# Optimization experiments

Measured on AMD Instinct MI355X. Metric: run time of the kernel, lower is better.

Reference implementation:

```python
import jax, jax.numpy as jnp
import numpy as np

NC, NS, NX, NZ = 128, 2048, 256, 512
B, K = 4, 1
NNZ = NX * NZ * NC  # 16_777_216 nonzeros (~Nc contributions per pixel)


def setup_inputs() -> dict:
    key = jax.random.key(0)
    k1, k2, k3, k4 = jax.random.split(key, 4)
    x = jax.random.normal(k1, (B, K, NC, NS), dtype=jnp.float32)
    csr_vals = jax.random.normal(k2, (NNZ,), dtype=jnp.float32)
    csr_rows = jnp.sort(jax.random.randint(k3, (NNZ,), 0, NX * NZ, dtype=jnp.int64))
    csr_cols = jax.random.randint(k4, (NNZ,), 0, NS * NC, dtype=jnp.int64)
    return {"x": x, "csr_vals": csr_vals, "csr_rows": csr_rows, "csr_cols": csr_cols}


def reference(x, csr_vals, csr_rows, csr_cols):
    # (B,K,Nc,Ns) -> (B,K,Ns,Nc) -> (B*K, Ns*Nc) -> transpose -> (Ns*Nc, B*K)
    rhs = jnp.transpose(x, (0, 1, 3, 2)).reshape(B * K, NS * NC).T
    # SpMM in COO form: out[r, :] += vals * rhs[cols, :]
    gathered = csr_vals[:, None] * rhs[csr_cols]          # (nnz, B*K)
    img_vec = jax.ops.segment_sum(gathered, csr_rows, num_segments=NX * NZ)  # (Nx*Nz, B*K)
    # transpose -> (B*K, Nx*Nz) -> (B,K,Nx,Nz) -> (B,K,Nz,Nx)
    return jnp.transpose(img_vec.T.reshape(B, K, NX, NZ), (0, 1, 3, 2))
```

## Files before the change

### kernel.cpp

```cpp
#include <hip/hip_runtime.h>
#include <hip/hip_fp16.h>

#define NC 128
#define NS 2048
#define NX 256
#define NZ 512
#define NROWS (NX * NZ)
#define NCOLS (NS * NC)
#define RUN 16
#define WAVE_NNZ (RUN * 64)
#define NSLOTS 64


struct alignas(8) Half4 { __half2 lo, hi; };

__global__ void pack_rhs_kernel(const float* __restrict__ x,
                                Half4* __restrict__ rhs) {
    int j = blockIdx.x * blockDim.x + threadIdx.x;
    if (j >= NCOLS) return;
    int c = j >> 11;
    int s = j & (NS - 1);
    int base = c * NS + s;
    Half4 h;
    h.lo = __float22half2_rn(make_float2(x[base],               x[base + 1 * NC * NS]));
    h.hi = __float22half2_rn(make_float2(x[base + 2 * NC * NS], x[base + 3 * NC * NS]));
    rhs[s * NC + c] = h;
}

__device__ __forceinline__ void global_flush(float* __restrict__ out, int r, float4 a) {
    int ix = r >> 9;
    int iz = r & (NZ - 1);
    int o = iz * NX + ix;
    atomicAdd(&out[0 * NROWS + o], a.x);
    atomicAdd(&out[1 * NROWS + o], a.y);
    atomicAdd(&out[2 * NROWS + o], a.z);
    atomicAdd(&out[3 * NROWS + o], a.w);
}

__global__ void __launch_bounds__(256, 4) spmm_seg_kernel(
        const float* __restrict__ vals,
        const int* __restrict__ cols,
        const int* __restrict__ rows,
        const Half4* __restrict__ rhs,
        float* __restrict__ out,
        int nnz) {
    __shared__ float sl[4][NSLOTS][4];

    int wv   = threadIdx.x >> 6;
    int lane = threadIdx.x & 63;
    int wid  = (blockIdx.x << 2) + wv;
    int base = wid * WAVE_NNZ + lane * RUN;

    ((float4*)sl)[threadIdx.x] = make_float4(0.f, 0.f, 0.f, 0.f);
    __syncthreads();

    float4 v[4];
    int4   c4[4], r4[4];
    if (base + RUN <= nnz) {
        #pragma unroll
        for (int q = 0; q < 4; ++q) c4[q] = *(const int4*)(cols + base + 4 * q);
        #pragma unroll
        for (int q = 0; q < 4; ++q) v[q]  = *(const float4*)(vals + base + 4 * q);
        #pragma unroll
        for (int q = 0; q < 4; ++q) r4[q] = *(const int4*)(rows + base + 4 * q);
    } else {
        #pragma unroll
        for (int q = 0; q < 4; ++q) {
            #pragma unroll
            for (int k = 0; k < 4; ++k) {
                int e = base + 4 * q + k;
                int ec = e < nnz ? e : (nnz - 1);
                (&v[q].x)[k]  = e < nnz ? vals[ec] : 0.f;
                (&c4[q].x)[k] = cols[ec];
                (&r4[q].x)[k] = rows[ec];
            }
        }
    }

    Half4 g[RUN];
    #pragma unroll
    for (int q = 0; q < 4; ++q) {
        g[4 * q + 0] = rhs[c4[q].x];
        g[4 * q + 1] = rhs[c4[q].y];
        g[4 * q + 2] = rhs[c4[q].z];
        g[4 * q + 3] = rhs[c4[q].w];
    }
    __builtin_amdgcn_sched_barrier(0);

    int rfirst = __shfl(r4[0].x, 0);
    int rlast  = __shfl(r4[3].w, 63);

    int cur = r4[0].x;
    float4 acc = make_float4(0.f, 0.f, 0.f, 0.f);
    #pragma unroll
    for (int j = 0; j < RUN; ++j) {
        int   rj = (&r4[j >> 2].x)[j & 3];
        float vj = (&v[j >> 2].x)[j & 3];
        float2 lo = __half22float2(g[j].lo);
        float2 hi = __half22float2(g[j].hi);
        if (rj != cur) {
            int s = cur - rfirst;
            if (s < NSLOTS) {
                atomicAdd(&sl[wv][s][0], acc.x);
                atomicAdd(&sl[wv][s][1], acc.y);
                atomicAdd(&sl[wv][s][2], acc.z);
                atomicAdd(&sl[wv][s][3], acc.w);
            } else {
                global_flush(out, cur, acc);
            }
            acc = make_float4(0.f, 0.f, 0.f, 0.f);
            cur = rj;
        }
        acc.x += vj * lo.x;
        acc.y += vj * lo.y;
        acc.z += vj * hi.x;
        acc.w += vj * hi.y;
    }
    {
        int s = cur - rfirst;
        if (s < NSLOTS) {
            atomicAdd(&sl[wv][s][0], acc.x);
            atomicAdd(&sl[wv][s][1], acc.y);
            atomicAdd(&sl[wv][s][2], acc.z);
            atomicAdd(&sl[wv][s][3], acc.w);
        } else {
            global_flush(out, cur, acc);
        }
    }

    __syncthreads();

    int span = rlast - rfirst;
    if (lane <= span && lane < NSLOTS) {
        float ax = sl[wv][lane][0];
        float ay = sl[wv][lane][1];
        float az = sl[wv][lane][2];
        float aw = sl[wv][lane][3];
        int rr = rfirst + lane;
        int ix = rr >> 9;
        int iz = rr & (NZ - 1);
        int o = iz * NX + ix;
        if (lane == 0 || rr == rlast) {
            atomicAdd(&out[0 * NROWS + o], ax);
            atomicAdd(&out[1 * NROWS + o], ay);
            atomicAdd(&out[2 * NROWS + o], az);
            atomicAdd(&out[3 * NROWS + o], aw);
        } else {
            out[0 * NROWS + o] = ax;
            out[1 * NROWS + o] = ay;
            out[2 * NROWS + o] = az;
            out[3 * NROWS + o] = aw;
        }
    }
}

__global__ void __launch_bounds__(256) spmm_direct_kernel(
        const float* __restrict__ x,
        const float* __restrict__ vals,
        const int* __restrict__ rows,
        const int* __restrict__ cols,
        int nnz,
        float* __restrict__ out) {
    int r = (blockIdx.x << 2) + (threadIdx.x >> 6);
    int lane = threadIdx.x & 63;
    int start, end;
    {
        int lo = 0, hi = nnz;
        while (lo < hi) { int mid = (lo + hi) >> 1; if (rows[mid] < r) lo = mid + 1; else hi = mid; }
        start = lo;
        hi = nnz;
        int key = r + 1;
        while (lo < hi) { int mid = (lo + hi) >> 1; if (rows[mid] < key) lo = mid + 1; else hi = mid; }
        end = lo;
    }
    float4 acc = {0.f, 0.f, 0.f, 0.f};
    for (int i = start + lane; i < end; i += 64) {
        float v = vals[i];
        int col = cols[i];
        int cc = col & (NC - 1);
        int ss = col >> 7;
        int b = cc * NS + ss;
        acc.x += v * x[b];
        acc.y += v * x[b + 1 * NC * NS];
        acc.z += v * x[b + 2 * NC * NS];
        acc.w += v * x[b + 3 * NC * NS];
    }
    #pragma unroll
    for (int off = 32; off >= 1; off >>= 1) {
        acc.x += __shfl_xor(acc.x, off, 64);
        acc.y += __shfl_xor(acc.y, off, 64);
        acc.z += __shfl_xor(acc.z, off, 64);
        acc.w += __shfl_xor(acc.w, off, 64);
    }
    if (lane < 4) {
        float o = (lane == 0) ? acc.x : (lane == 1) ? acc.y : (lane == 2) ? acc.z : acc.w;
        int ix = r >> 9;
        int iz = r & (NZ - 1);
        out[lane * NROWS + iz * NX + ix] = o;
    }
}

extern "C" void kernel_launch(void* const* d_in, const int* in_sizes, int n_in,
                              void* d_out, int out_size, void* d_ws, size_t ws_size,
                              hipStream_t stream) {
    const float* x        = (const float*)d_in[0];
    const float* csr_vals = (const float*)d_in[1];
    const int*   csr_rows = (const int*)d_in[2];
    const int*   csr_cols = (const int*)d_in[3];
    float* out = (float*)d_out;
    int nnz = in_sizes[1];

    size_t need = (size_t)NCOLS * sizeof(Half4);
    if (ws_size >= need) {
        Half4* rhs = (Half4*)d_ws;
        hipMemsetAsync(out, 0, (size_t)out_size * sizeof(float), stream);
        pack_rhs_kernel<<<(NCOLS + 255) / 256, 256, 0, stream>>>(x, rhs);
        int nblocks = (nnz + 4 * WAVE_NNZ - 1) / (4 * WAVE_NNZ);
        spmm_seg_kernel<<<nblocks, 256, 0, stream>>>(csr_vals, csr_cols, csr_rows,
                                                     rhs, out, nnz);
    } else {
        spmm_direct_kernel<<<NROWS / 4, 256, 0, stream>>>(x, csr_vals, csr_rows, csr_cols, nnz, out);
    }
}
```

Measured before the change: 283.3 us.

## Software-pipeline SpMM gathers across four tiles per wave with inline-asm loads

```diff
diff --git a/kernel.cpp b/kernel.cpp
--- a/kernel.cpp
+++ b/kernel.cpp
@@ -7,12 +7,36 @@
 #define NZ 512
 #define NROWS (NX * NZ)
 #define NCOLS (NS * NC)
-#define RUN 16
-#define WAVE_NNZ (RUN * 64)
+#define RUN 8
+#define TILE_NNZ (RUN * 64)
+#define NT 4
+#define WAVE_RANGE (NT * TILE_NNZ)
 #define NSLOTS 64
 
 
 struct alignas(8) Half4 { __half2 lo, hi; };
+
+typedef int   vi4 __attribute__((ext_vector_type(4)));
+typedef float vf4 __attribute__((ext_vector_type(4)));
+
+__device__ __forceinline__ void ld4i(vi4& d, const int* p) {
+    asm volatile("global_load_dwordx4 %0, %1, off"
+                 : "=v"(d) : "v"((unsigned long long)p));
+}
+__device__ __forceinline__ void ld4f(vf4& d, const float* p) {
+    asm volatile("global_load_dwordx4 %0, %1, off"
+                 : "=v"(d) : "v"((unsigned long long)p));
+}
+__device__ __forceinline__ void ld1i(int& d, const int* p) {
+    asm volatile("global_load_dword %0, %1, off"
+                 : "=v"(d) : "v"((unsigned long long)p));
+}
+__device__ __forceinline__ void ld2u(unsigned long long& d, const Half4* p) {
+    asm volatile("global_load_dwordx2 %0, %1, off"
+                 : "=v"(d) : "v"((unsigned long long)p));
+}
+#define WAITV(n) do { asm volatile("s_waitcnt vmcnt(" #n ")" ::: "memory"); \
+                      __builtin_amdgcn_sched_barrier(0); } while (0)
 
 __global__ void pack_rhs_kernel(const float* __restrict__ x,
                                 Half4* __restrict__ rhs) {
@@ -37,7 +61,55 @@
     atomicAdd(&out[3 * NROWS + o], a.w);
 }
 
-__global__ void __launch_bounds__(256, 4) spmm_seg_kernel(
+__device__ __forceinline__ void flush_slot(float (*slw)[4], int rfirst, int cur,
+                                           float4 acc, float* __restrict__ out) {
+    int s = cur - rfirst;
+    if (s < NSLOTS) {
+        atomicAdd(&slw[s][0], acc.x);
+        atomicAdd(&slw[s][1], acc.y);
+        atomicAdd(&slw[s][2], acc.z);
+        atomicAdd(&slw[s][3], acc.w);
+    } else {
+        global_flush(out, cur, acc);
+    }
+}
+
+__device__ __forceinline__ void accum8(const vf4& va, const vf4& vb,
+                                       const vi4& ra, const vi4& rb,
+                                       const unsigned long long (&g)[8],
+                                       int rfirst, int& cur, float4& acc,
+                                       float* __restrict__ out, float (*slw)[4]) {
+    #pragma unroll
+    for (int j = 0; j < 8; ++j) {
+        int   rj = (j < 4) ? ra[j] : rb[j - 4];
+        float vj = (j < 4) ? va[j] : vb[j - 4];
+        union { unsigned long long u; Half4 h; } u; u.u = g[j];
+        float2 lo = __half22float2(u.h.lo);
+        float2 hi = __half22float2(u.h.hi);
+        if (rj != cur) {
+            flush_slot(slw, rfirst, cur, acc, out);
+            acc = make_float4(0.f, 0.f, 0.f, 0.f);
+            cur = rj;
+        }
+        acc.x += vj * lo.x;
+        acc.y += vj * lo.y;
+        acc.z += vj * hi.x;
+        acc.w += vj * hi.y;
+    }
+}
+
+#define ISSUE_S(cx0, cx1, vx0, vx1, rx0, rx1, b) do { \
+    ld4i(cx0, cols + (b));     ld4i(cx1, cols + (b) + 4); \
+    ld4f(vx0, vals + (b));     ld4f(vx1, vals + (b) + 4); \
+    ld4i(rx0, rows + (b));     ld4i(rx1, rows + (b) + 4); } while (0)
+
+#define ISSUE_G(g, c0, c1) do { \
+    ld2u(g[0], rhs + (c0).x);  ld2u(g[1], rhs + (c0).y); \
+    ld2u(g[2], rhs + (c0).z);  ld2u(g[3], rhs + (c0).w); \
+    ld2u(g[4], rhs + (c1).x);  ld2u(g[5], rhs + (c1).y); \
+    ld2u(g[6], rhs + (c1).z);  ld2u(g[7], rhs + (c1).w); } while (0)
+
+__global__ void __launch_bounds__(256, 5) spmm_pipe_kernel(
         const float* __restrict__ vals,
         const int* __restrict__ cols,
         const int* __restrict__ rows,
@@ -49,107 +121,124 @@
     int wv   = threadIdx.x >> 6;
     int lane = threadIdx.x & 63;
     int wid  = (blockIdx.x << 2) + wv;
-    int base = wid * WAVE_NNZ + lane * RUN;
-
-    ((float4*)sl)[threadIdx.x] = make_float4(0.f, 0.f, 0.f, 0.f);
-    __syncthreads();
-
-    float4 v[4];
-    int4   c4[4], r4[4];
-    if (base + RUN <= nnz) {
-        #pragma unroll
-        for (int q = 0; q < 4; ++q) c4[q] = *(const int4*)(cols + base + 4 * q);
-        #pragma unroll
-        for (int q = 0; q < 4; ++q) v[q]  = *(const float4*)(vals + base + 4 * q);
-        #pragma unroll
-        for (int q = 0; q < 4; ++q) r4[q] = *(const int4*)(rows + base + 4 * q);
-    } else {
-        #pragma unroll
-        for (int q = 0; q < 4; ++q) {
-            #pragma unroll
-            for (int k = 0; k < 4; ++k) {
-                int e = base + 4 * q + k;
-                int ec = e < nnz ? e : (nnz - 1);
-                (&v[q].x)[k]  = e < nnz ? vals[ec] : 0.f;
-                (&c4[q].x)[k] = cols[ec];
-                (&r4[q].x)[k] = rows[ec];
+    int wstart = wid * WAVE_RANGE;
+    if (wstart >= nnz) return;
+
+    float (*slw)[4] = sl[wv];
+    *(float4*)(&slw[lane][0]) = make_float4(0.f, 0.f, 0.f, 0.f);
+
+    if (wstart + WAVE_RANGE <= nnz) {
+        const int b0 = wstart + 0 * TILE_NNZ + lane * RUN;
+        const int b1 = wstart + 1 * TILE_NNZ + lane * RUN;
+        const int b2 = wstart + 2 * TILE_NNZ + lane * RUN;
+        const int b3 = wstart + 3 * TILE_NNZ + lane * RUN;
+
+        int rf, rl;
+        vi4 cA0, cA1, cB0, cB1;
+        vf4 vA0, vA1, vB0, vB1;
+        vi4 rA0, rA1, rB0, rB1;
+        unsigned long long gA[8], gB[8];
+
+        ld1i(rf, rows + wstart);
+        ld1i(rl, rows + wstart + WAVE_RANGE - 1);
+        ld4i(cA0, cols + b0); ld4i(cA1, cols + b0 + 4);
+        ld4f(vA0, vals + b0); ld4f(vA1, vals + b0 + 4);
+        ld4i(rA0, rows + b0); ld4i(rA1, rows + b0 + 4);
+        WAITV(4);
+        ISSUE_G(gA, cA0, cA1);
+        ISSUE_S(cB0, cB1, vB0, vB1, rB0, rB1, b1);
+        WAITV(14);
+        WAITV(6);
+
+        int cur = rf;
+        float4 acc = make_float4(0.f, 0.f, 0.f, 0.f);
+
+        accum8(vA0, vA1, rA0, rA1, gA, rf, cur, acc, out, slw);
+        WAITV(4);
+        ISSUE_G(gB, cB0, cB1);
+        ISSUE_S(cA0, cA1, vA0, vA1, rA0, rA1, b2);
+        WAITV(14);
+        WAITV(6);
+
+        accum8(vB0, vB1, rB0, rB1, gB, rf, cur, acc, out, slw);
+        WAITV(4);
+        ISSUE_G(gA, cA0, cA1);
+        ISSUE_S(cB0, cB1, vB0, vB1, rB0, rB1, b3);
+        WAITV(14);
+        WAITV(6);
+
+        accum8(vA0, vA1, rA0, rA1, gA, rf, cur, acc, out, slw);
+        WAITV(4);
+        ISSUE_G(gB, cB0, cB1);
+        WAITV(8);
+        WAITV(0);
+
+        accum8(vB0, vB1, rB0, rB1, gB, rf, cur, acc, out, slw);
+
+        flush_slot(slw, rf, cur, acc, out);
+
+        int span = rl - rf;
+        if (lane <= span && lane < NSLOTS) {
+            float ax = slw[lane][0];
+            float ay = slw[lane][1];
+            float az = slw[lane][2];
+            float aw = slw[lane][3];
+            int rr = rf + lane;
+            int ix = rr >> 9;
+            int iz = rr & (NZ - 1);
+            int o = iz * NX + ix;
+            if (lane == 0 || rr == rl) {
+                atomicAdd(&out[0 * NROWS + o], ax);
+                atomicAdd(&out[1 * NROWS + o], ay);
+                atomicAdd(&out[2 * NROWS + o], az);
+                atomicAdd(&out[3 * NROWS + o], aw);
+            } else {
+                out[0 * NROWS + o] = ax;
+                out[1 * NROWS + o] = ay;
+                out[2 * NROWS + o] = az;
+                out[3 * NROWS + o] = aw;
             }
         }
-    }
-
-    Half4 g[RUN];
-    #pragma unroll
-    for (int q = 0; q < 4; ++q) {
-        g[4 * q + 0] = rhs[c4[q].x];
-        g[4 * q + 1] = rhs[c4[q].y];
-        g[4 * q + 2] = rhs[c4[q].z];
-        g[4 * q + 3] = rhs[c4[q].w];
-    }
-    __builtin_amdgcn_sched_barrier(0);
-
-    int rfirst = __shfl(r4[0].x, 0);
-    int rlast  = __shfl(r4[3].w, 63);
-
-    int cur = r4[0].x;
-    float4 acc = make_float4(0.f, 0.f, 0.f, 0.f);
-    #pragma unroll
-    for (int j = 0; j < RUN; ++j) {
-        int   rj = (&r4[j >> 2].x)[j & 3];
-        float vj = (&v[j >> 2].x)[j & 3];
-        float2 lo = __half22float2(g[j].lo);
-        float2 hi = __half22float2(g[j].hi);
-        if (rj != cur) {
-            int s = cur - rfirst;
-            if (s < NSLOTS) {
-                atomicAdd(&sl[wv][s][0], acc.x);
-                atomicAdd(&sl[wv][s][1], acc.y);
-                atomicAdd(&sl[wv][s][2], acc.z);
-                atomicAdd(&sl[wv][s][3], acc.w);
-            } else {
-                global_flush(out, cur, acc);
+    } else {
+        int wend = nnz;
+        int rf = rows[wstart];
+        int rl = rows[wend - 1];
+        int cur = rf;
+        float4 acc = make_float4(0.f, 0.f, 0.f, 0.f);
+        for (int t = 0; t < NT; ++t) {
+            int tb = wstart + t * TILE_NNZ + lane * RUN;
+            #pragma unroll
+            for (int j = 0; j < RUN; ++j) {
+                int e = tb + j;
+                if (e >= nnz) break;
+                float vj = vals[e];
+                int   cj = cols[e];
+                int   rj = rows[e];
+                Half4 h = rhs[cj];
+                float2 lo = __half22float2(h.lo);
+                float2 hi = __half22float2(h.hi);
+                if (rj != cur) {
+                    flush_slot(slw, rf, cur, acc, out);
+                    acc = make_float4(0.f, 0.f, 0.f, 0.f);
+                    cur = rj;
+                }
+                acc.x += vj * lo.x;
+                acc.y += vj * lo.y;
+                acc.z += vj * hi.x;
+                acc.w += vj * hi.y;
             }
-            acc = make_float4(0.f, 0.f, 0.f, 0.f);
-            cur = rj;
         }
-        acc.x += vj * lo.x;
-        acc.y += vj * lo.y;
-        acc.z += vj * hi.x;
-        acc.w += vj * hi.y;
-    }
-    {
-        int s = cur - rfirst;
-        if (s < NSLOTS) {
-            atomicAdd(&sl[wv][s][0], acc.x);
-            atomicAdd(&sl[wv][s][1], acc.y);
-            atomicAdd(&sl[wv][s][2], acc.z);
-            atomicAdd(&sl[wv][s][3], acc.w);
-        } else {
-            global_flush(out, cur, acc);
-        }
-    }
-
-    __syncthreads();
-
-    int span = rlast - rfirst;
-    if (lane <= span && lane < NSLOTS) {
-        float ax = sl[wv][lane][0];
-        float ay = sl[wv][lane][1];
-        float az = sl[wv][lane][2];
-        float aw = sl[wv][lane][3];
-        int rr = rfirst + lane;
-        int ix = rr >> 9;
-        int iz = rr & (NZ - 1);
-        int o = iz * NX + ix;
-        if (lane == 0 || rr == rlast) {
-            atomicAdd(&out[0 * NROWS + o], ax);
-            atomicAdd(&out[1 * NROWS + o], ay);
-            atomicAdd(&out[2 * NROWS + o], az);
-            atomicAdd(&out[3 * NROWS + o], aw);
-        } else {
-            out[0 * NROWS + o] = ax;
-            out[1 * NROWS + o] = ay;
-            out[2 * NROWS + o] = az;
-            out[3 * NROWS + o] = aw;
+        flush_slot(slw, rf, cur, acc, out);
+        int span = rl - rf;
+        if (lane <= span && lane < NSLOTS) {
+            int rr = rf + lane;
+            int ix = rr >> 9;
+            int iz = rr & (NZ - 1);
+            int o = iz * NX + ix;
+            atomicAdd(&out[0 * NROWS + o], slw[lane][0]);
+            atomicAdd(&out[1 * NROWS + o], slw[lane][1]);
+            atomicAdd(&out[2 * NROWS + o], slw[lane][2]);
+            atomicAdd(&out[3 * NROWS + o], slw[lane][3]);
         }
     }
 }
@@ -215,9 +304,10 @@
         Half4* rhs = (Half4*)d_ws;
         hipMemsetAsync(out, 0, (size_t)out_size * sizeof(float), stream);
         pack_rhs_kernel<<<(NCOLS + 255) / 256, 256, 0, stream>>>(x, rhs);
-        int nblocks = (nnz + 4 * WAVE_NNZ - 1) / (4 * WAVE_NNZ);
-        spmm_seg_kernel<<<nblocks, 256, 0, stream>>>(csr_vals, csr_cols, csr_rows,
-                                                     rhs, out, nnz);
+        int per_block = 4 * WAVE_RANGE;
+        int nblocks = (nnz + per_block - 1) / per_block;
+        spmm_pipe_kernel<<<nblocks, 256, 0, stream>>>(csr_vals, csr_cols, csr_rows,
+                                                      rhs, out, nnz);
     } else {
         spmm_direct_kernel<<<NROWS / 4, 256, 0, stream>>>(x, csr_vals, csr_rows, csr_cols, nnz, out);
     }
```

After: 297.0 us. 4.9% more time.
